# Optimization experiments

Measured on AMD Instinct MI355X. Metric: run time of the kernel, lower is better.

Reference implementation:

```python
import jax, jax.numpy as jnp
import numpy as np

EPS = 1e-5  # torch LayerNorm default
DT_RANK = 32  # ceil(d_model=512 / 16)


def layer_norm(x, g, b):
    mu = x.mean(-1, keepdims=True)
    var = x.var(-1, keepdims=True)
    return (x - mu) / jnp.sqrt(var + EPS) * g + b


def conv1d(x, w, b, pad):
    # x: (B, C, L), w: (O, I, K) -- torch Conv1d semantics
    y = jax.lax.conv_general_dilated(x, w, (1,), [(pad, pad)],
                                     dimension_numbers=('NCH', 'OIH', 'NCH'))
    return y + b[None, :, None]


def mamba(u, in_w, conv_w, conv_b, xproj_w, dt_w, dt_b, Alog, D, out_w, d_state, d_conv):
    # Faithful mamba_ssm Mamba block (no biases on in/x/out proj, RMS of official impl)
    Bsz, L, _ = u.shape
    xz = jnp.einsum('bld,ed->ble', u, in_w)          # (B, L, 2*Di)
    x, z = jnp.split(xz, 2, axis=-1)
    Di = x.shape[-1]
    # causal depthwise conv1d, truncated to L (padding=d_conv-1 on the left)
    xc = jax.lax.conv_general_dilated(x.transpose(0, 2, 1), conv_w[:, None, :], (1,),
                                      [(d_conv - 1, 0)],
                                      dimension_numbers=('NCH', 'OIH', 'NCH'),
                                      feature_group_count=Di)
    x = jax.nn.silu((xc + conv_b[None, :, None]).transpose(0, 2, 1))  # (B, L, Di)
    xdb = jnp.einsum('bld,ed->ble', x, xproj_w)       # (B, L, dt_rank + 2*N)
    dt = jax.nn.softplus(jnp.einsum('blr,dr->bld', xdb[..., :DT_RANK], dt_w) + dt_b)
    Bm = xdb[..., DT_RANK:DT_RANK + d_state]          # (B, L, N)
    Cm = xdb[..., DT_RANK + d_state:]                 # (B, L, N)
    A = -jnp.exp(Alog)                                # (Di, N)

    def step(h, ins):
        dt_t, x_t, B_t, C_t = ins                     # (B,Di),(B,Di),(B,N),(B,N)
        dA = jnp.exp(dt_t[..., None] * A)             # (B, Di, N)
        h = dA * h + (dt_t * x_t)[..., None] * B_t[:, None, :]
        y = (h * C_t[:, None, :]).sum(-1)             # (B, Di)
        return h, y

    h0 = jnp.zeros((Bsz, Di, d_state), u.dtype)
    xs = (dt.transpose(1, 0, 2), x.transpose(1, 0, 2),
          Bm.transpose(1, 0, 2), Cm.transpose(1, 0, 2))
    _, ys = jax.lax.scan(step, h0, xs)
    y = ys.transpose(1, 0, 2) + x * D                 # skip via D
    y = y * jax.nn.silu(z)
    return jnp.einsum('bld,od->blo', y, out_w)


def _forward(x, fe_w, fe_b, fe_ln_g, fe_ln_b, emb_ln_g, emb_ln_b,
             conv1_w, conv1_b, conv2_w, conv2_b,
             mf_in_w, mf_conv_w, mf_conv_b, mf_xproj_w, mf_dt_w, mf_dt_b, mf_Alog, mf_D, mf_out_w,
             mb_in_w, mb_conv_w, mb_conv_b, mb_xproj_w, mb_dt_w, mb_dt_b, mb_Alog, mb_D, mb_out_w,
             norm_g, norm_b, fc1_w, fc1_b, fc2_w, fc2_b):
    x = x.reshape(x.shape[0], 100, 23)
    # FrequencyEmbedding: rfft over a length-1 last dim == the signal itself; |.| then Linear+LN+ReLU
    id_mag = jnp.abs(x[..., :1])                      # (B, 100, 1)
    e = jax.nn.relu(layer_norm(id_mag @ fe_w.T + fe_b, fe_ln_g, fe_ln_b))
    id_embed = jax.nn.relu(layer_norm(e, emb_ln_g, emb_ln_b))  # outer LN+ReLU
    data = x[..., 1:].transpose(0, 2, 1)              # (B, 22, 100)
    f1 = jax.nn.relu(conv1d(data, conv1_w, conv1_b, 1))
    f2 = jax.nn.relu(conv1d(f1, conv2_w, conv2_b, 1)).transpose(0, 2, 1)  # (B,100,256)
    comb = jnp.concatenate([id_embed, f2], axis=-1)   # (B, 100, 512)
    fo = mamba(comb, mf_in_w, mf_conv_w, mf_conv_b, mf_xproj_w, mf_dt_w, mf_dt_b,
               mf_Alog, mf_D, mf_out_w, 16, 4)
    bo = mamba(comb[:, ::-1], mb_in_w, mb_conv_w, mb_conv_b, mb_xproj_w, mb_dt_w, mb_dt_b,
               mb_Alog, mb_D, mb_out_w, 8, 2)[:, ::-1]
    pooled = (fo + bo).max(axis=1)                    # (B, 512)
    pooled = layer_norm(pooled, norm_g, norm_b)       # self.norm (undefined in source; LN(512))
    h = jax.nn.relu(pooled @ fc1_w.T + fc1_b)
    return h @ fc2_w.T + fc2_b                        # (B, 4)


def setup_inputs() -> dict:
    key = jax.random.key(0)
    ks = iter(jax.random.split(key, 48))
    def n(shape, s=0.02):
        return jax.random.normal(next(ks), shape, jnp.float32) * s
    Di = 1024
    alog16 = jnp.log(jnp.tile(jnp.arange(1, 17, dtype=jnp.float32), (Di, 1)))
    alog8 = jnp.log(jnp.tile(jnp.arange(1, 9, dtype=jnp.float32), (Di, 1)))
    return {
        'x': jax.random.normal(next(ks), (512, 2300), jnp.float32),
        'fe_w': n((256, 1), 1.0), 'fe_b': jnp.zeros(256, jnp.float32),
        'fe_ln_g': jnp.ones(256, jnp.float32), 'fe_ln_b': jnp.zeros(256, jnp.float32),
        'emb_ln_g': jnp.ones(256, jnp.float32), 'emb_ln_b': jnp.zeros(256, jnp.float32),
        'conv1_w': n((128, 22, 3)), 'conv1_b': jnp.zeros(128, jnp.float32),
        'conv2_w': n((256, 128, 3)), 'conv2_b': jnp.zeros(256, jnp.float32),
        'mf_in_w': n((2 * Di, 512)), 'mf_conv_w': n((Di, 4)), 'mf_conv_b': jnp.zeros(Di, jnp.float32),
        'mf_xproj_w': n((32 + 2 * 16, Di)), 'mf_dt_w': n((Di, 32)), 'mf_dt_b': n((Di,), 0.1),
        'mf_Alog': alog16, 'mf_D': jnp.ones(Di, jnp.float32), 'mf_out_w': n((512, Di)),
        'mb_in_w': n((2 * Di, 512)), 'mb_conv_w': n((Di, 2)), 'mb_conv_b': jnp.zeros(Di, jnp.float32),
        'mb_xproj_w': n((32 + 2 * 8, Di)), 'mb_dt_w': n((Di, 32)), 'mb_dt_b': n((Di,), 0.1),
        'mb_Alog': alog8, 'mb_D': jnp.ones(Di, jnp.float32), 'mb_out_w': n((512, Di)),
        'norm_g': jnp.ones(512, jnp.float32), 'norm_b': jnp.zeros(512, jnp.float32),
        'fc1_w': n((128, 512)), 'fc1_b': jnp.zeros(128, jnp.float32),
        'fc2_w': n((4, 128)), 'fc2_b': jnp.zeros(4, jnp.float32),
    }


def reference(x, fe_w, fe_b, fe_ln_g, fe_ln_b, emb_ln_g, emb_ln_b,
              conv1_w, conv1_b, conv2_w, conv2_b,
              mf_in_w, mf_conv_w, mf_conv_b, mf_xproj_w, mf_dt_w, mf_dt_b, mf_Alog, mf_D, mf_out_w,
              mb_in_w, mb_conv_w, mb_conv_b, mb_xproj_w, mb_dt_w, mb_dt_b, mb_Alog, mb_D, mb_out_w,
              norm_g, norm_b, fc1_w, fc1_b, fc2_w, fc2_b):
    return _forward(x, fe_w, fe_b, fe_ln_g, fe_ln_b, emb_ln_g, emb_ln_b,
                    conv1_w, conv1_b, conv2_w, conv2_b,
                    mf_in_w, mf_conv_w, mf_conv_b, mf_xproj_w, mf_dt_w, mf_dt_b, mf_Alog, mf_D, mf_out_w,
                    mb_in_w, mb_conv_w, mb_conv_b, mb_xproj_w, mb_dt_w, mb_dt_b, mb_Alog, mb_D, mb_out_w,
                    norm_g, norm_b, fc1_w, fc1_b, fc2_w, fc2_b)
```

## Files before the change

kernel.cpp:

```cpp
#include <hip/hip_runtime.h>
#include <cstddef>
#include <cstdint>

#define BSZ 512
#define SEQ 100

typedef __bf16 bf16_t;
typedef __attribute__((ext_vector_type(8))) __bf16 bf16x8;
typedef __attribute__((ext_vector_type(4))) float f32x4;

__device__ __forceinline__ float sigmoidf_(float v){ return 1.f/(1.f + __expf(-v)); }
__device__ __forceinline__ float siluf_(float v){ return v * sigmoidf_(v); }
__device__ __forceinline__ float softplusf_(float v){ return (v > 20.f) ? v : __logf(1.f + __expf(v)); }

__global__ __launch_bounds__(256) void cvt_bf16_kernel(
    const float* __restrict__ src, bf16_t* __restrict__ dst, int n)
{
    int i = blockIdx.x*256 + threadIdx.x;
    if (i < n) dst[i] = (bf16_t)src[i];
}

__global__ __launch_bounds__(256) void prep_outw_kernel(
    const float* __restrict__ of, const float* __restrict__ ob, bf16_t* __restrict__ W)
{
    int i = blockIdx.x*256 + threadIdx.x;
    if (i < 512*2048){
        int o = i >> 11, k = i & 2047;
        W[i] = (bf16_t)((k < 1024) ? of[o*1024 + k] : ob[o*1024 + (k - 1024)]);
    }
}

__global__ __launch_bounds__(256) void prep_convw_kernel(
    const float* __restrict__ c1w, const float* __restrict__ c2w,
    bf16_t* __restrict__ W1p, bf16_t* __restrict__ W2p)
{
    int i = blockIdx.x*256 + threadIdx.x;
    if (i < 128*96){
        int o = i / 96, kk = i - o*96, k = kk >> 5, c = kk & 31;
        W1p[i] = (c < 22) ? (bf16_t)c1w[(o*22 + c)*3 + k] : (bf16_t)0.f;
    }
    if (i < 256*384){
        int o = i / 384, kk = i - o*384, k = kk >> 7, c = kk & 127;
        W2p[i] = (bf16_t)c2w[(o*128 + c)*3 + k];
    }
}

__global__ __launch_bounds__(256) void fe0_kernel(
    const float* __restrict__ x,
    const float* __restrict__ fe_w, const float* __restrict__ fe_b,
    const float* __restrict__ g1, const float* __restrict__ b1,
    const float* __restrict__ g2, const float* __restrict__ b2,
    bf16_t* __restrict__ comb, bf16_t* __restrict__ F0pad, bf16_t* __restrict__ F1pad)
{
    const int b = blockIdx.x;
    const int t = threadIdx.x;
    const int wv = t >> 6, lane = t & 63;

    float few[4], feb[4], lg1[4], lb1[4], lg2[4], lb2[4];
    #pragma unroll
    for (int q = 0; q < 4; ++q){
        int j = lane + 64*q;
        few[q] = fe_w[j]; feb[q] = fe_b[j];
        lg1[q] = g1[j];  lb1[q] = b1[j];
        lg2[q] = g2[j];  lb2[q] = b2[j];
    }
    for (int l = wv; l < SEQ; l += 4){
        float m = fabsf(x[(size_t)(b*SEQ + l)*23]);
        float e[4];
        float s1 = 0.f, s2 = 0.f;
        #pragma unroll
        for (int q = 0; q < 4; ++q){ e[q] = m*few[q] + feb[q]; s1 += e[q]; s2 += e[q]*e[q]; }
        #pragma unroll
        for (int off = 32; off > 0; off >>= 1){ s1 += __shfl_xor(s1, off); s2 += __shfl_xor(s2, off); }
        float mean = s1 * (1.f/256.f);
        float rstd = rsqrtf(s2*(1.f/256.f) - mean*mean + 1e-5f);
        s1 = 0.f; s2 = 0.f;
        #pragma unroll
        for (int q = 0; q < 4; ++q){
            e[q] = fmaxf((e[q]-mean)*rstd*lg1[q] + lb1[q], 0.f);
            s1 += e[q]; s2 += e[q]*e[q];
        }
        #pragma unroll
        for (int off = 32; off > 0; off >>= 1){ s1 += __shfl_xor(s1, off); s2 += __shfl_xor(s2, off); }
        mean = s1 * (1.f/256.f);
        rstd = rsqrtf(s2*(1.f/256.f) - mean*mean + 1e-5f);
        #pragma unroll
        for (int q = 0; q < 4; ++q){
            float v = fmaxf((e[q]-mean)*rstd*lg2[q] + lb2[q], 0.f);
            comb[(size_t)(b*SEQ + l)*512 + lane + 64*q] = (bf16_t)v;
        }
    }

    for (int idx = t; idx < 102*32; idx += 256){
        int r = idx >> 5, c = idx & 31;
        float v = 0.f;
        if (r >= 1 && r <= SEQ && c < 22) v = x[(size_t)(b*SEQ + r - 1)*23 + 1 + c];
        F0pad[(size_t)(b*102 + r)*32 + c] = (bf16_t)v;
    }
    if (t < 128) F1pad[(size_t)(b*102 + 0)*128 + t] = (bf16_t)0.f;
    else F1pad[(size_t)(b*102 + 101)*128 + (t - 128)] = (bf16_t)0.f;
}

__global__ __launch_bounds__(256) void gemm_conv_kernel(
    const bf16_t* __restrict__ Abase, int lda, int Az,
    const bf16_t* __restrict__ W, int K, int N,
    const float* __restrict__ bias,
    bf16_t* __restrict__ Cbase, int ldc, int Cb, int coff, int noff, int Mtot)
{
    __shared__ bf16_t As[128*32];
    __shared__ bf16_t Ws[128*32];
    const bf16_t* A = Abase + (size_t)blockIdx.z * Az;
    const int t = threadIdx.x;
    const int lane = t & 63, w = t >> 6;
    const int n0 = blockIdx.y * 128;
    const int rsub = lane >> 2, csub = lane & 3;
    const int col = lane & 15, quad = lane >> 4;
    const int wOffM = (w & 1) * 64, wOffN = (w >> 1) * 64;

    f32x4 acc[4][4];
    #pragma unroll
    for (int i = 0; i < 4; ++i)
        #pragma unroll
        for (int j = 0; j < 4; ++j)
            acc[i][j] = (f32x4){0.f, 0.f, 0.f, 0.f};

    for (int k0 = 0; k0 < K; k0 += 32){
        __syncthreads();
        #pragma unroll
        for (int q = 0; q < 2; ++q){
            const int rt = w*32 + q*16 + rsub;
            const int lq = csub ^ ((rt >> 1) & 3);
            int ra = (rt < Mtot) ? rt : (Mtot - 1);
            const bf16_t* ga = A + (size_t)ra*lda + k0 + lq*8;
            __builtin_amdgcn_global_load_lds(
                (const __attribute__((address_space(1))) void*)ga,
                (__attribute__((address_space(3))) void*)&As[(w*32 + q*16)*32], 16, 0, 0);
            const bf16_t* gw = W + (size_t)(n0 + rt)*K + k0 + lq*8;
            __builtin_amdgcn_global_load_lds(
                (const __attribute__((address_space(1))) void*)gw,
                (__attribute__((address_space(3))) void*)&Ws[(w*32 + q*16)*32], 16, 0, 0);
        }
        __syncthreads();

        bf16x8 af[4], bfv[4];
        #pragma unroll
        for (int i = 0; i < 4; ++i){
            const int ra = wOffM + i*16 + col;
            af[i]  = *(const bf16x8*)&As[ra*32 + (quad ^ ((ra >> 1) & 3))*8];
            const int rb = wOffN + i*16 + col;
            bfv[i] = *(const bf16x8*)&Ws[rb*32 + (quad ^ ((rb >> 1) & 3))*8];
        }
        #pragma unroll
        for (int i = 0; i < 4; ++i)
            #pragma unroll
            for (int j = 0; j < 4; ++j)
                acc[i][j] = __builtin_amdgcn_mfma_f32_16x16x32_bf16(af[i], bfv[j], acc[i][j], 0, 0, 0);
    }

    #pragma unroll
    for (int i = 0; i < 4; ++i){
        const int gmb = wOffM + i*16 + quad*4;
        #pragma unroll
        for (int j = 0; j < 4; ++j){
            const int gn = n0 + wOffN + j*16 + col;
            const float bb = bias[gn];
            #pragma unroll
            for (int r = 0; r < 4; ++r){
                const int gm = gmb + r;
                if (gm < Mtot){
                    float v = fmaxf(acc[i][j][r] + bb, 0.f);
                    Cbase[((size_t)blockIdx.z*Cb + coff + gm)*ldc + noff + gn] = (bf16_t)v;
                }
            }
        }
    }
}

__global__ __launch_bounds__(256) void gemm_in_kernel(
    const bf16_t* __restrict__ A, int lda, int Mtot,
    const bf16_t* __restrict__ W, int K,
    bf16_t* __restrict__ xy, bf16_t* __restrict__ z)
{
    __shared__ bf16_t smem[128*132];
    bf16_t* As0 = smem;
    bf16_t* As1 = smem + 4096;
    bf16_t* Ws0 = smem + 8192;
    bf16_t* Ws1 = smem + 12288;
    const int t = threadIdx.x;
    const int lane = t & 63, w = t >> 6;
    const int m0 = blockIdx.x * 128, n0 = blockIdx.y * 128;
    const int rsub = lane >> 2, csub = lane & 3;
    const int col = lane & 15, quad = lane >> 4;
    const int wOffM = (w & 1) * 64, wOffN = (w >> 1) * 64;

    f32x4 acc[4][4];
    #pragma unroll
    for (int i = 0; i < 4; ++i)
        #pragma unroll
        for (int j = 0; j < 4; ++j)
            acc[i][j] = (f32x4){0.f, 0.f, 0.f, 0.f};

    for (int k0 = 0; k0 < K; k0 += 64){
        __syncthreads();
        #pragma unroll
        for (int hh = 0; hh < 2; ++hh){
            bf16_t* Asb = hh ? As1 : As0;
            bf16_t* Wsb = hh ? Ws1 : Ws0;
            #pragma unroll
            for (int q = 0; q < 2; ++q){
                const int rt = w*32 + q*16 + rsub;
                const int lq = csub ^ ((rt >> 1) & 3);
                int ra = m0 + rt; ra = (ra < Mtot) ? ra : (Mtot - 1);
                const bf16_t* ga = A + (size_t)ra*lda + k0 + hh*32 + lq*8;
                __builtin_amdgcn_global_load_lds(
                    (const __attribute__((address_space(1))) void*)ga,
                    (__attribute__((address_space(3))) void*)&Asb[(w*32 + q*16)*32], 16, 0, 0);
                const bf16_t* gw = W + (size_t)(n0 + rt)*K + k0 + hh*32 + lq*8;
                __builtin_amdgcn_global_load_lds(
                    (const __attribute__((address_space(1))) void*)gw,
                    (__attribute__((address_space(3))) void*)&Wsb[(w*32 + q*16)*32], 16, 0, 0);
            }
        }
        __syncthreads();

        #pragma unroll
        for (int hh = 0; hh < 2; ++hh){
            bf16_t* Asb = hh ? As1 : As0;
            bf16_t* Wsb = hh ? Ws1 : Ws0;
            bf16x8 af[4], bfv[4];
            #pragma unroll
            for (int i = 0; i < 4; ++i){
                const int ra = wOffM + i*16 + col;
                af[i]  = *(const bf16x8*)&Asb[ra*32 + (quad ^ ((ra >> 1) & 3))*8];
                const int rb = wOffN + i*16 + col;
                bfv[i] = *(const bf16x8*)&Wsb[rb*32 + (quad ^ ((rb >> 1) & 3))*8];
            }
            #pragma unroll
            for (int i = 0; i < 4; ++i)
                #pragma unroll
                for (int j = 0; j < 4; ++j)
                    acc[i][j] = __builtin_amdgcn_mfma_f32_16x16x32_bf16(af[i], bfv[j], acc[i][j], 0, 0, 0);
        }
    }

    __syncthreads();
    #pragma unroll
    for (int i = 0; i < 4; ++i){
        const int row0 = wOffM + i*16 + quad*4;
        #pragma unroll
        for (int j = 0; j < 4; ++j){
            const int cT = wOffN + j*16 + col;
            #pragma unroll
            for (int r = 0; r < 4; ++r)
                smem[(row0 + r)*132 + cT] = (bf16_t)acc[i][j][r];
        }
    }
    __syncthreads();

    const int half = n0 >> 11, within = n0 & 2047;
    bf16_t* dstBase = ((within < 1024) ? xy : z) + half*1024 + (within & 1023);
    #pragma unroll
    for (int k = 0; k < 8; ++k){
        const int idx = t + k*256;
        const int row = idx >> 4;
        const int ch  = (idx & 15) * 8;
        const int gm = m0 + row;
        if (gm < Mtot)
            *(bf16x8*)&dstBase[(size_t)gm*2048 + ch] = *(const bf16x8*)&smem[row*132 + ch];
    }
}

__global__ __launch_bounds__(256) void gemm_out_kernel(
    const bf16_t* __restrict__ A, int Mtot,
    const bf16_t* __restrict__ W,
    float* __restrict__ C)
{
    __shared__ bf16_t As[2][128*32];
    __shared__ bf16_t Ws[2][128*32];
    const int t = threadIdx.x;
    const int lane = t & 63, w = t >> 6;
    const int m0 = blockIdx.x * 128, n0 = blockIdx.y * 128;
    const int rsub = lane >> 2, csub = lane & 3;
    const int col = lane & 15, quad = lane >> 4;
    const int wOffM = (w & 1) * 64, wOffN = (w >> 1) * 64;
    const int K = 2048;

    f32x4 acc[4][4];
    #pragma unroll
    for (int i = 0; i < 4; ++i)
        #pragma unroll
        for (int j = 0; j < 4; ++j)
            acc[i][j] = (f32x4){0.f, 0.f, 0.f, 0.f};

    for (int k0 = 0; k0 < K; k0 += 64){
        __syncthreads();
        #pragma unroll
        for (int hh = 0; hh < 2; ++hh){
            #pragma unroll
            for (int q = 0; q < 2; ++q){
                const int rt = w*32 + q*16 + rsub;
                const int lq = csub ^ ((rt >> 1) & 3);
                int ra = m0 + rt; ra = (ra < Mtot) ? ra : (Mtot - 1);
                const bf16_t* ga = A + (size_t)ra*K + k0 + hh*32 + lq*8;
                __builtin_amdgcn_global_load_lds(
                    (const __attribute__((address_space(1))) void*)ga,
                    (__attribute__((address_space(3))) void*)&As[hh][(w*32 + q*16)*32], 16, 0, 0);
                const bf16_t* gw = W + (size_t)(n0 + rt)*K + k0 + hh*32 + lq*8;
                __builtin_amdgcn_global_load_lds(
                    (const __attribute__((address_space(1))) void*)gw,
                    (__attribute__((address_space(3))) void*)&Ws[hh][(w*32 + q*16)*32], 16, 0, 0);
            }
        }
        __syncthreads();

        #pragma unroll
        for (int hh = 0; hh < 2; ++hh){
            bf16x8 af[4], bfv[4];
            #pragma unroll
            for (int i = 0; i < 4; ++i){
                const int ra = wOffM + i*16 + col;
                af[i]  = *(const bf16x8*)&As[hh][ra*32 + (quad ^ ((ra >> 1) & 3))*8];
                const int rb = wOffN + i*16 + col;
                bfv[i] = *(const bf16x8*)&Ws[hh][rb*32 + (quad ^ ((rb >> 1) & 3))*8];
            }
            #pragma unroll
            for (int i = 0; i < 4; ++i)
                #pragma unroll
                for (int j = 0; j < 4; ++j)
                    acc[i][j] = __builtin_amdgcn_mfma_f32_16x16x32_bf16(af[i], bfv[j], acc[i][j], 0, 0, 0);
        }
    }

    #pragma unroll
    for (int i = 0; i < 4; ++i){
        const int gmb = m0 + wOffM + i*16 + quad*4;
        #pragma unroll
        for (int j = 0; j < 4; ++j){
            const int gn = n0 + wOffN + j*16 + col;
            #pragma unroll
            for (int r = 0; r < 4; ++r){
                const int gm = gmb + r;
                if (gm < Mtot)
                    C[(size_t)gm*512 + gn] = acc[i][j][r];
            }
        }
    }
}

__global__ __launch_bounds__(256) void gemm_x_kernel(
    const bf16_t* __restrict__ xc,
    const bf16_t* __restrict__ Wf, const bf16_t* __restrict__ Wb,
    float* __restrict__ C)
{
    __shared__ bf16_t As[128*32];
    __shared__ bf16_t Ws[64*32];
    const int half = blockIdx.y;
    const bf16_t* A = xc + half*1024;
    const bf16_t* W = half ? Wb : Wf;
    const int N = half ? 48 : 64;
    const int t = threadIdx.x;
    const int lane = t & 63, w = t >> 6;
    const int m0 = blockIdx.x * 128;
    const int rsub = lane >> 2, csub = lane & 3;
    const int col = lane & 15, quad = lane >> 4;

    f32x4 acc[2][4];
    #pragma unroll
    for (int i = 0; i < 2; ++i)
        #pragma unroll
        for (int j = 0; j < 4; ++j)
            acc[i][j] = (f32x4){0.f, 0.f, 0.f, 0.f};

    for (int k0 = 0; k0 < 1024; k0 += 32){
        __syncthreads();
        #pragma unroll
        for (int q = 0; q < 2; ++q){
            const int rt = q*64 + w*16 + rsub;
            const int lq = csub ^ ((rt >> 1) & 3);
            const bf16_t* ga = A + (size_t)(m0 + rt)*2048 + k0 + lq*8;
            __builtin_amdgcn_global_load_lds(
                (const __attribute__((address_space(1))) void*)ga,
                (__attribute__((address_space(3))) void*)&As[(q*64 + w*16)*32], 16, 0, 0);
        }
        {
            const int rt = w*16 + rsub;
            const int lq = csub ^ ((rt >> 1) & 3);
            int rw = (rt < N) ? rt : (N - 1);
            const bf16_t* gw = W + (size_t)rw*1024 + k0 + lq*8;
            __builtin_amdgcn_global_load_lds(
                (const __attribute__((address_space(1))) void*)gw,
                (__attribute__((address_space(3))) void*)&Ws[(w*16)*32], 16, 0, 0);
        }
        __syncthreads();

        bf16x8 af[2], bfv[4];
        #pragma unroll
        for (int i = 0; i < 2; ++i){
            const int ra = w*32 + i*16 + col;
            af[i]  = *(const bf16x8*)&As[ra*32 + (quad ^ ((ra >> 1) & 3))*8];
        }
        #pragma unroll
        for (int j = 0; j < 4; ++j){
            const int rb = j*16 + col;
            bfv[j] = *(const bf16x8*)&Ws[rb*32 + (quad ^ ((rb >> 1) & 3))*8];
        }
        #pragma unroll
        for (int i = 0; i < 2; ++i)
            #pragma unroll
            for (int j = 0; j < 4; ++j)
                acc[i][j] = __builtin_amdgcn_mfma_f32_16x16x32_bf16(af[i], bfv[j], acc[i][j], 0, 0, 0);
    }

    #pragma unroll
    for (int i = 0; i < 2; ++i){
        const int gmb = m0 + w*32 + i*16 + quad*4;
        #pragma unroll
        for (int j = 0; j < 4; ++j){
            const int gn = j*16 + col;
            if (gn < N){
                #pragma unroll
                for (int r = 0; r < 4; ++r)
                    C[(size_t)(gmb + r)*128 + half*64 + gn] = acc[i][j][r];
            }
        }
    }
}

__global__ __launch_bounds__(256) void dt_kernel(
    const float* __restrict__ xdb,
    const float* __restrict__ dtwf, const float* __restrict__ dtbf,
    const float* __restrict__ dtwb, const float* __restrict__ dtbb,
    bf16_t* __restrict__ dto)
{
    const int half = blockIdx.y >> 3;
    const int d = (blockIdx.y & 7)*128 + (threadIdx.x & 127);
    const int mslot = threadIdx.x >> 7;
    const int m0 = blockIdx.x * 16;
    __shared__ float sd[16*32];
    for (int i = threadIdx.x; i < 16*32; i += 256){
        int r = i >> 5, c = i & 31;
        sd[i] = xdb[(size_t)(m0 + r)*128 + half*64 + c];
    }
    const float* dw = half ? dtwb : dtwf;
    float w[32];
    #pragma unroll
    for (int r = 0; r < 32; ++r) w[r] = dw[d*32 + r];
    const float db = half ? dtbb[d] : dtbf[d];
    __syncthreads();
    #pragma unroll
    for (int i = 0; i < 8; ++i){
        const int row = mslot + i*2;
        const float* rp = &sd[row*32];
        float a = db;
        #pragma unroll
        for (int r = 0; r < 32; ++r) a += w[r]*rp[r];
        dto[(size_t)(m0 + row)*2048 + half*1024 + d] = (bf16_t)softplusf_(a);
    }
}

__global__ __launch_bounds__(256) void conv_silu_kernel(
    const bf16_t* __restrict__ xin,
    bf16_t* __restrict__ xout,
    const float* __restrict__ cwf, const float* __restrict__ cbf,
    const float* __restrict__ cwb, const float* __restrict__ cbb)
{
    const int gid = blockIdx.x*256 + threadIdx.x;
    const int d2 = gid & 2047;
    const int rest = gid >> 11;
    const int b = rest / 10;
    const int g = rest - b*10;
    const int l0 = g*10;
    const int half = d2 >> 10, d = d2 & 1023;
    const bf16_t* in = xin + (size_t)b*SEQ*2048 + d2;
    bf16_t* outp = xout + (size_t)b*SEQ*2048 + d2;

    if (half == 0){
        const float w0 = cwf[d*4], w1 = cwf[d*4+1], w2 = cwf[d*4+2], w3 = cwf[d*4+3];
        const float bias = cbf[d];
        float v[13];
        #pragma unroll
        for (int i = 0; i < 13; ++i){
            const int l = l0 - 3 + i;
            v[i] = (l >= 0) ? (float)in[(size_t)l*2048] : 0.f;
        }
        #pragma unroll
        for (int i = 0; i < 10; ++i){
            const float a = bias + w0*v[i] + w1*v[i+1] + w2*v[i+2] + w3*v[i+3];
            outp[(size_t)(l0+i)*2048] = (bf16_t)siluf_(a);
        }
    } else {
        const float w0 = cwb[d*2], w1 = cwb[d*2+1];
        const float bias = cbb[d];
        float v[11];
        #pragma unroll
        for (int i = 0; i < 11; ++i){
            const int l = l0 + i;
            v[i] = (l < SEQ) ? (float)in[(size_t)l*2048] : 0.f;
        }
        #pragma unroll
        for (int i = 0; i < 10; ++i){
            const float a = bias + w1*v[i] + w0*v[i+1];
            outp[(size_t)(l0+i)*2048] = (bf16_t)siluf_(a);
        }
    }
}

template<int DSS, int ROW, bool REV>
__device__ __forceinline__ void scan2_core(
    bf16_t* __restrict__ xcb,
    const bf16_t* __restrict__ tb,
    const bf16_t* __restrict__ zb,
    const float* __restrict__ sxB,
    const float* __restrict__ sxC,
    const float* __restrict__ Av, float Dd, bool wr)
{
    float h[DSS];
    #pragma unroll
    for (int j = 0; j < DSS; ++j) h[j] = 0.f;
    const int step = REV ? -1 : 1;
    int l = REV ? (SEQ-1) : 0;

    #pragma unroll 1
    for (int blk = 0; blk < 10; ++blk){
        float xr[10], zr[10], tr[10];
        #pragma unroll
        for (int i = 0; i < 10; ++i){
            const size_t li = (size_t)(l + step*i);
            xr[i] = (float)xcb[li*2048];
            zr[i] = (float)zb[li*2048];
            tr[i] = (float)tb[li*2048];
        }
        #pragma unroll
        for (int i = 0; i < 10; ++i){
            const int li = l + step*i;
            const float dtv = tr[i];
            const float dtx = dtv * xr[i];
            const float* Bp = &sxB[li*ROW];
            const float* Cp = &sxC[li*ROW];
            float yv = 0.f;
            #pragma unroll
            for (int j = 0; j < DSS; ++j){
                h[j] = __expf(dtv*Av[j])*h[j] + dtx*Bp[j];
                yv += h[j]*Cp[j];
            }
            yv += __shfl_xor(yv, 1);
            yv += __shfl_xor(yv, 2);
            yv += xr[i]*Dd;
            yv *= siluf_(zr[i]);
            if (wr) xcb[(size_t)li*2048] = (bf16_t)yv;
        }
        l += step*10;
    }
}

__global__ __launch_bounds__(256) void scan_kernel(
    bf16_t* __restrict__ xc,
    const bf16_t* __restrict__ dtv,
    const bf16_t* __restrict__ z,
    const float* __restrict__ xdb,
    const float* __restrict__ Alogf, const float* __restrict__ Dpf,
    const float* __restrict__ Alogb, const float* __restrict__ Dpb)
{
    const int b = blockIdx.x >> 5, k = blockIdx.x & 31;
    const int t = threadIdx.x;
    const int sub = t & 3, chl = t >> 2;
    const bool fwd = (k < 16);

    __shared__ float sx[SEQ*32];
    const float4* src = (const float4*)(xdb + (size_t)b*SEQ*128);
    if (fwd){
        float4* dst = (float4*)sx;
        for (int i = t; i < SEQ*8; i += 256){
            int row = i >> 3, c = i & 7;
            dst[row*8 + c] = src[row*32 + 8 + c];
        }
    } else {
        float4* dst = (float4*)sx;
        for (int i = t; i < SEQ*4; i += 256){
            int row = i >> 2, c = i & 3;
            dst[row*4 + c] = src[row*32 + 24 + c];
        }
    }
    __syncthreads();

    const bool wr = (sub == 0);
    if (fwd){
        const int d = k*64 + chl;
        const size_t off = (size_t)b*SEQ*2048 + d;
        float Av[4];
        #pragma unroll
        for (int j = 0; j < 4; ++j) Av[j] = -__expf(Alogf[d*16 + sub*4 + j]);
        scan2_core<4, 32, false>(xc + off, dtv + off, z + off,
                                 sx + sub*4, sx + 16 + sub*4, Av, Dpf[d], wr);
    } else {
        const int d = (k - 16)*64 + chl;
        const size_t off = (size_t)b*SEQ*2048 + 1024 + d;
        float Av[2];
        #pragma unroll
        for (int j = 0; j < 2; ++j) Av[j] = -__expf(Alogb[d*8 + sub*2 + j]);
        scan2_core<2, 16, true>(xc + off, dtv + off, z + off,
                                sx + sub*2, sx + 8 + sub*2, Av, Dpb[d], wr);
    }
}

__global__ __launch_bounds__(256) void pool_kernel(
    const float* __restrict__ acc,
    float* __restrict__ pooled)
{
    const int b = blockIdx.x, y = blockIdx.y;
    const int c = y*128 + (threadIdx.x & 127);
    const int half = threadIdx.x >> 7;
    const float* base = acc + (size_t)b*SEQ*512 + c;
    float m = -3.4e38f;
    #pragma unroll 5
    for (int l = half*50; l < half*50 + 50; ++l)
        m = fmaxf(m, base[(size_t)l*512]);
    __shared__ float sm[256];
    sm[threadIdx.x] = m;
    __syncthreads();
    if (half == 0)
        pooled[(size_t)b*512 + c] = fmaxf(sm[threadIdx.x], sm[threadIdx.x + 128]);
}

__global__ __launch_bounds__(256) void head_kernel(
    const float* __restrict__ pooled,
    const float* __restrict__ ng, const float* __restrict__ nb,
    const float* __restrict__ w1, const float* __restrict__ b1,
    const float* __restrict__ w2, const float* __restrict__ b2,
    float* __restrict__ out)
{
    const int b = blockIdx.x, t = threadIdx.x;
    __shared__ float sp[512];
    __shared__ float sh2[256];
    __shared__ float sh[128];
    __shared__ float red1[4], red2[4];

    float s1 = 0.f, s2 = 0.f;
    for (int o = t; o < 512; o += 256){
        float v = pooled[(size_t)b*512 + o];
        sp[o] = v; s1 += v; s2 += v*v;
    }
    #pragma unroll
    for (int off = 32; off > 0; off >>= 1){ s1 += __shfl_xor(s1, off); s2 += __shfl_xor(s2, off); }
    const int wv = t >> 6, lane = t & 63;
    if (lane == 0){ red1[wv] = s1; red2[wv] = s2; }
    __syncthreads();
    if (t == 0){
        float a = 0.f, c = 0.f;
        for (int i = 0; i < 4; ++i){ a += red1[i]; c += red2[i]; }
        float mean = a * (1.f/512.f);
        float var = c * (1.f/512.f) - mean*mean;
        red1[0] = mean; red2[0] = rsqrtf(var + 1e-5f);
    }
    __syncthreads();
    const float mean = red1[0], rstd = red2[0];
    for (int o = t; o < 512; o += 256) sp[o] = (sp[o]-mean)*rstd*ng[o] + nb[o];
    __syncthreads();

    {
        const int o = t & 127, half = t >> 7;
        const float4* wrow = (const float4*)(w1 + (size_t)o*512 + half*256);
        const float4* sp4 = (const float4*)sp + half*64;
        float s = 0.f;
        #pragma unroll 8
        for (int j = 0; j < 64; ++j){
            float4 a = sp4[j], wq = wrow[j];
            s += a.x*wq.x + a.y*wq.y + a.z*wq.z + a.w*wq.w;
        }
        sh2[t] = s;
    }
    __syncthreads();
    if (t < 128) sh[t] = fmaxf(sh2[t] + sh2[t + 128] + b1[t], 0.f);
    __syncthreads();
    if (t < 4){
        float a = b2[t];
        for (int j = 0; j < 128; ++j) a += sh[j]*w2[t*128 + j];
        out[b*4 + t] = a;
    }
}

extern "C" void kernel_launch(void* const* d_in, const int* in_sizes, int n_in,
                              void* d_out, int out_size, void* d_ws, size_t ws_size,
                              hipStream_t stream)
{
    (void)in_sizes; (void)n_in; (void)out_size;
    const float* x        = (const float*)d_in[0];
    const float* fe_w     = (const float*)d_in[1];
    const float* fe_b     = (const float*)d_in[2];
    const float* fe_ln_g  = (const float*)d_in[3];
    const float* fe_ln_b  = (const float*)d_in[4];
    const float* emb_ln_g = (const float*)d_in[5];
    const float* emb_ln_b = (const float*)d_in[6];
    const float* conv1_w  = (const float*)d_in[7];
    const float* conv1_b  = (const float*)d_in[8];
    const float* conv2_w  = (const float*)d_in[9];
    const float* conv2_b  = (const float*)d_in[10];
    const float* mf_in_w  = (const float*)d_in[11];
    const float* mf_conv_w= (const float*)d_in[12];
    const float* mf_conv_b= (const float*)d_in[13];
    const float* mf_xproj = (const float*)d_in[14];
    const float* mf_dt_w  = (const float*)d_in[15];
    const float* mf_dt_b  = (const float*)d_in[16];
    const float* mf_Alog  = (const float*)d_in[17];
    const float* mf_D     = (const float*)d_in[18];
    const float* mf_out_w = (const float*)d_in[19];
    const float* mb_in_w  = (const float*)d_in[20];
    const float* mb_conv_w= (const float*)d_in[21];
    const float* mb_conv_b= (const float*)d_in[22];
    const float* mb_xproj = (const float*)d_in[23];
    const float* mb_dt_w  = (const float*)d_in[24];
    const float* mb_dt_b  = (const float*)d_in[25];
    const float* mb_Alog  = (const float*)d_in[26];
    const float* mb_D     = (const float*)d_in[27];
    const float* mb_out_w = (const float*)d_in[28];
    const float* norm_g   = (const float*)d_in[29];
    const float* norm_b   = (const float*)d_in[30];
    const float* fc1_w    = (const float*)d_in[31];
    const float* fc1_b    = (const float*)d_in[32];
    const float* fc2_w    = (const float*)d_in[33];
    const float* fc2_b    = (const float*)d_in[34];
    float* out = (float*)d_out;

    char* p = (char*)d_ws;
    bf16_t* w_in   = (bf16_t*)p; p += (size_t)4096*512*sizeof(bf16_t);
    bf16_t* w_out  = (bf16_t*)p; p += (size_t)512*2048*sizeof(bf16_t);
    bf16_t* w_xpf  = (bf16_t*)p; p += (size_t)64*1024*sizeof(bf16_t);
    bf16_t* w_xpb  = (bf16_t*)p; p += (size_t)48*1024*sizeof(bf16_t);
    bf16_t* W1p    = (bf16_t*)p; p += (size_t)128*96*sizeof(bf16_t);
    bf16_t* W2p    = (bf16_t*)p; p += (size_t)256*384*sizeof(bf16_t);
    bf16_t* comb_all = (bf16_t*)p; p += (size_t)BSZ*SEQ*512*sizeof(bf16_t);
    const size_t fixed_bytes = (size_t)(p - (char*)d_ws);

    const size_t per_b = (size_t)SEQ * (2048*2 + 2048*2 + 2048*2 + 128*4);
    const size_t budget = (ws_size > fixed_bytes) ? (ws_size - fixed_bytes) : 0;
    int Bc = BSZ;
    while (Bc > 64 && (size_t)Bc * per_b > budget) Bc >>= 1;
    const int nch = BSZ / Bc;
    const int M = Bc * SEQ;

    bf16_t* F0pad = (bf16_t*)p;
    bf16_t* F1pad = F0pad + (size_t)BSZ*102*32;
    bf16_t* xy   = (bf16_t*)p;               p += (size_t)M*2048*sizeof(bf16_t);
    bf16_t* z    = (bf16_t*)p;               p += (size_t)M*2048*sizeof(bf16_t);
    bf16_t* dtb  = (bf16_t*)p;               p += (size_t)M*2048*sizeof(bf16_t);
    float*  xdb  = (float*)p;
    float*  accb = (float*)xy;

    cvt_bf16_kernel<<<(2048*512+255)/256, 256, 0, stream>>>(mf_in_w, w_in, 2048*512);
    cvt_bf16_kernel<<<(2048*512+255)/256, 256, 0, stream>>>(mb_in_w, w_in + (size_t)2048*512, 2048*512);
    prep_outw_kernel<<<(512*2048+255)/256, 256, 0, stream>>>(mf_out_w, mb_out_w, w_out);
    cvt_bf16_kernel<<<(64*1024+255)/256,  256, 0, stream>>>(mf_xproj, w_xpf, 64*1024);
    cvt_bf16_kernel<<<(48*1024+255)/256,  256, 0, stream>>>(mb_xproj, w_xpb, 48*1024);
    prep_convw_kernel<<<(256*384+255)/256, 256, 0, stream>>>(conv1_w, conv2_w, W1p, W2p);

    fe0_kernel<<<BSZ, 256, 0, stream>>>(x, fe_w, fe_b, fe_ln_g, fe_ln_b,
        emb_ln_g, emb_ln_b, comb_all, F0pad, F1pad);
    gemm_conv_kernel<<<dim3(1, 1, BSZ), 256, 0, stream>>>(
        F0pad, 32, 102*32, W1p, 96, 128, conv1_b, F1pad, 128, 102, 1, 0, SEQ);
    gemm_conv_kernel<<<dim3(1, 2, BSZ), 256, 0, stream>>>(
        F1pad, 128, 102*128, W2p, 384, 256, conv2_b, comb_all, 512, 100, 0, 256, SEQ);

    const int gm128 = M / 128;

    for (int c = 0; c < nch; ++c){
        const size_t b0 = (size_t)c * Bc;
        const bf16_t* comb = comb_all + b0*SEQ*512;

        gemm_in_kernel<<<dim3(gm128, 32), 256, 0, stream>>>(comb, 512, M, w_in, 512, xy, z);
        conv_silu_kernel<<<Bc*80, 256, 0, stream>>>(xy, dtb, mf_conv_w, mf_conv_b,
                                                    mb_conv_w, mb_conv_b);
        gemm_x_kernel<<<dim3(gm128, 2), 256, 0, stream>>>(dtb, w_xpf, w_xpb, xdb);
        dt_kernel<<<dim3(M/16, 16), 256, 0, stream>>>(xdb, mf_dt_w, mf_dt_b,
                                                      mb_dt_w, mb_dt_b, xy);
        scan_kernel<<<Bc*32, 256, 0, stream>>>(dtb, xy, z, xdb,
                                               mf_Alog, mf_D, mb_Alog, mb_D);
        gemm_out_kernel<<<dim3(gm128, 4), 256, 0, stream>>>(dtb, M, w_out, accb);
        pool_kernel<<<dim3(Bc, 4), 256, 0, stream>>>(accb, xdb);
        head_kernel<<<Bc, 256, 0, stream>>>(xdb, norm_g, norm_b, fc1_w, fc1_b,
                                            fc2_w, fc2_b, out + b0*4);
    }
}
```

Before: 1.791 ms.

## Stage scan inputs through LDS in chunks with packed x/dt loads

The selective-scan kernel now cooperatively loads 25-timestep chunks of x, dt and z into shared memory, packing x and dt into one 32-bit word. This replaces the per-thread strided global loads that were repeated by all four sub-threads of each channel. B and C coefficients are read as vector loads from shared memory. The cost is extra barriers per chunk and additional LDS usage, which may lower occupancy.

Result: slower. 1.829 ms (+2.2%).

```diff
diff --git a/kernel.cpp b/kernel.cpp
--- a/kernel.cpp
+++ b/kernel.cpp
@@ -8,6 +8,8 @@
 typedef __bf16 bf16_t;
 typedef __attribute__((ext_vector_type(8))) __bf16 bf16x8;
 typedef __attribute__((ext_vector_type(4))) float f32x4;
+typedef __attribute__((ext_vector_type(2))) float f32x2;
+typedef unsigned short ushort_t;
 
 __device__ __forceinline__ float sigmoidf_(float v){ return 1.f/(1.f + __expf(-v)); }
 __device__ __forceinline__ float siluf_(float v){ return v * sigmoidf_(v); }
@@ -506,50 +508,72 @@
 }
 
 template<int DSS, int ROW, bool REV>
-__device__ __forceinline__ void scan2_core(
-    bf16_t* __restrict__ xcb,
-    const bf16_t* __restrict__ tb,
-    const bf16_t* __restrict__ zb,
-    const float* __restrict__ sxB,
-    const float* __restrict__ sxC,
-    const float* __restrict__ Av, float Dd, bool wr)
-{
+__device__ __forceinline__ void scan3_core(
+    const ushort_t* __restrict__ xcB,
+    const ushort_t* __restrict__ dtB,
+    const ushort_t* __restrict__ zB,
+    bf16_t* __restrict__ yB,
+    const float* __restrict__ sx,
+    uint32_t* __restrict__ sxdt, ushort_t* __restrict__ szs,
+    const float* __restrict__ Av, float Dd)
+{
+    const int t = threadIdx.x;
+    const int sub = t & 3, chl = t >> 2;
+    const bool wrr = (sub == 0);
     float h[DSS];
     #pragma unroll
     for (int j = 0; j < DSS; ++j) h[j] = 0.f;
-    const int step = REV ? -1 : 1;
-    int l = REV ? (SEQ-1) : 0;
 
     #pragma unroll 1
-    for (int blk = 0; blk < 10; ++blk){
-        float xr[10], zr[10], tr[10];
-        #pragma unroll
-        for (int i = 0; i < 10; ++i){
-            const size_t li = (size_t)(l + step*i);
-            xr[i] = (float)xcb[li*2048];
-            zr[i] = (float)zb[li*2048];
-            tr[i] = (float)tb[li*2048];
-        }
-        #pragma unroll
-        for (int i = 0; i < 10; ++i){
-            const int li = l + step*i;
-            const float dtv = tr[i];
-            const float dtx = dtv * xr[i];
-            const float* Bp = &sxB[li*ROW];
-            const float* Cp = &sxC[li*ROW];
+    for (int q = 0; q < 4; ++q){
+        __syncthreads();
+        for (int idx = t; idx < 25*64; idx += 256){
+            const int r = idx >> 6, ch = idx & 63;
+            const int s = q*25 + r;
+            const int gl = REV ? (SEQ-1 - s) : s;
+            const size_t off = (size_t)gl*2048 + ch;
+            const uint32_t px = xcB[off];
+            const uint32_t pt = dtB[off];
+            sxdt[idx] = px | (pt << 16);
+            szs[idx]  = zB[off];
+        }
+        __syncthreads();
+        int li = REV ? (SEQ-1 - q*25) : q*25;
+        const int stp = REV ? -1 : 1;
+        #pragma unroll 5
+        for (int r = 0; r < 25; ++r){
+            const uint32_t p = sxdt[r*64 + chl];
+            const float xv   = __uint_as_float(p << 16);
+            const float dtvv = __uint_as_float(p & 0xffff0000u);
+            const float dtx  = dtvv * xv;
             float yv = 0.f;
-            #pragma unroll
-            for (int j = 0; j < DSS; ++j){
-                h[j] = __expf(dtv*Av[j])*h[j] + dtx*Bp[j];
-                yv += h[j]*Cp[j];
+            if (DSS == 4){
+                const f32x4 Bv = *(const f32x4*)&sx[li*ROW + sub*4];
+                const f32x4 Cv = *(const f32x4*)&sx[li*ROW + ROW/2 + sub*4];
+                #pragma unroll
+                for (int j = 0; j < 4; ++j){
+                    h[j] = __expf(dtvv*Av[j])*h[j] + dtx*Bv[j];
+                    yv += h[j]*Cv[j];
+                }
+            } else {
+                const f32x2 Bv = *(const f32x2*)&sx[li*ROW + sub*2];
+                const f32x2 Cv = *(const f32x2*)&sx[li*ROW + ROW/2 + sub*2];
+                #pragma unroll
+                for (int j = 0; j < 2; ++j){
+                    h[j] = __expf(dtvv*Av[j])*h[j] + dtx*Bv[j];
+                    yv += h[j]*Cv[j];
+                }
             }
             yv += __shfl_xor(yv, 1);
             yv += __shfl_xor(yv, 2);
-            yv += xr[i]*Dd;
-            yv *= siluf_(zr[i]);
-            if (wr) xcb[(size_t)li*2048] = (bf16_t)yv;
-        }
-        l += step*10;
+            if (wrr){
+                const float zv = __uint_as_float(((uint32_t)szs[r*64 + chl]) << 16);
+                float y = yv + xv*Dd;
+                y *= siluf_(zv);
+                yB[(size_t)li*2048] = (bf16_t)y;
+            }
+            li += stp;
+        }
     }
 }
 
@@ -567,6 +591,9 @@
     const bool fwd = (k < 16);
 
     __shared__ float sx[SEQ*32];
+    __shared__ uint32_t sxdt[25*64];
+    __shared__ ushort_t szs[25*64];
+
     const float4* src = (const float4*)(xdb + (size_t)b*SEQ*128);
     if (fwd){
         float4* dst = (float4*)sx;
@@ -581,25 +608,31 @@
             dst[row*4 + c] = src[row*32 + 24 + c];
         }
     }
-    __syncthreads();
-
-    const bool wr = (sub == 0);
+
     if (fwd){
-        const int d = k*64 + chl;
-        const size_t off = (size_t)b*SEQ*2048 + d;
+        const int d0 = k*64;
+        const int d = d0 + chl;
+        const size_t boff = (size_t)b*SEQ*2048 + d0;
         float Av[4];
         #pragma unroll
         for (int j = 0; j < 4; ++j) Av[j] = -__expf(Alogf[d*16 + sub*4 + j]);
-        scan2_core<4, 32, false>(xc + off, dtv + off, z + off,
-                                 sx + sub*4, sx + 16 + sub*4, Av, Dpf[d], wr);
+        scan3_core<4, 32, false>((const ushort_t*)xc + boff,
+                                 (const ushort_t*)dtv + boff,
+                                 (const ushort_t*)z + boff,
+                                 xc + boff + chl,
+                                 sx, sxdt, szs, Av, Dpf[d]);
     } else {
-        const int d = (k - 16)*64 + chl;
-        const size_t off = (size_t)b*SEQ*2048 + 1024 + d;
+        const int d0 = (k - 16)*64;
+        const int d = d0 + chl;
+        const size_t boff = (size_t)b*SEQ*2048 + 1024 + d0;
         float Av[2];
         #pragma unroll
         for (int j = 0; j < 2; ++j) Av[j] = -__expf(Alogb[d*8 + sub*2 + j]);
-        scan2_core<2, 16, true>(xc + off, dtv + off, z + off,
-                                sx + sub*2, sx + 8 + sub*2, Av, Dpb[d], wr);
+        scan3_core<2, 16, true>((const ushort_t*)xc + boff,
+                                (const ushort_t*)dtv + boff,
+                                (const ushort_t*)z + boff,
+                                xc + boff + chl,
+                                sx, sxdt, szs, Av, Dpb[d]);
     }
 }
 
```

## Restructure selective scan: one thread per channel, staged windows, geometric exp recurrence

Applied to the files above, without the earlier changes.

The scan kernel now gives each thread a whole channel's state (16 forward or 8 backward) instead of splitting it across 4 lanes with shuffles, and launches 8 blocks per batch row that handle both directions. Each 10-step window of x, dt and z is staged cooperatively through shared memory with coalesced 32-bit loads. At runtime the kernel checks whether A[j] = (j+1)*A[0] (the S4D-real init); if so it computes one exp and builds the other decay factors by repeated multiplication, and otherwise it falls back to per-state exps. This cuts transcendental work and shuffles, at the cost of fewer blocks, more registers, extra barriers, and small rounding drift from the chained products.

New measurement: 1.537 ms. 1.16x faster.

```diff
diff --git a/kernel.cpp b/kernel.cpp
--- a/kernel.cpp
+++ b/kernel.cpp
@@ -8,6 +8,7 @@
 typedef __bf16 bf16_t;
 typedef __attribute__((ext_vector_type(8))) __bf16 bf16x8;
 typedef __attribute__((ext_vector_type(4))) float f32x4;
+typedef unsigned short ushort_t;
 
 __device__ __forceinline__ float sigmoidf_(float v){ return 1.f/(1.f + __expf(-v)); }
 __device__ __forceinline__ float siluf_(float v){ return v * sigmoidf_(v); }
@@ -505,52 +506,44 @@
     }
 }
 
-template<int DSS, int ROW, bool REV>
-__device__ __forceinline__ void scan2_core(
-    bf16_t* __restrict__ xcb,
-    const bf16_t* __restrict__ tb,
-    const bf16_t* __restrict__ zb,
-    const float* __restrict__ sxB,
-    const float* __restrict__ sxC,
-    const float* __restrict__ Av, float Dd, bool wr)
-{
-    float h[DSS];
-    #pragma unroll
-    for (int j = 0; j < DSS; ++j) h[j] = 0.f;
-    const int step = REV ? -1 : 1;
-    int l = REV ? (SEQ-1) : 0;
-
-    #pragma unroll 1
-    for (int blk = 0; blk < 10; ++blk){
-        float xr[10], zr[10], tr[10];
-        #pragma unroll
-        for (int i = 0; i < 10; ++i){
-            const size_t li = (size_t)(l + step*i);
-            xr[i] = (float)xcb[li*2048];
-            zr[i] = (float)zb[li*2048];
-            tr[i] = (float)tb[li*2048];
-        }
-        #pragma unroll
-        for (int i = 0; i < 10; ++i){
-            const int li = l + step*i;
-            const float dtv = tr[i];
-            const float dtx = dtv * xr[i];
-            const float* Bp = &sxB[li*ROW];
-            const float* Cp = &sxC[li*ROW];
-            float yv = 0.f;
-            #pragma unroll
-            for (int j = 0; j < DSS; ++j){
-                h[j] = __expf(dtv*Av[j])*h[j] + dtx*Bp[j];
-                yv += h[j]*Cp[j];
-            }
-            yv += __shfl_xor(yv, 1);
-            yv += __shfl_xor(yv, 2);
-            yv += xr[i]*Dd;
-            yv *= siluf_(zr[i]);
-            if (wr) xcb[(size_t)li*2048] = (bf16_t)yv;
-        }
-        l += step*10;
-    }
+template<int DS>
+__device__ __forceinline__ float scan_step_struct(
+    float* __restrict__ h, float A0, float dtv_, float dtx, const float4* __restrict__ sxl4)
+{
+    const float rr = __expf(dtv_*A0);
+    const float r2 = rr*rr;
+    float rb = rr;
+    float y0 = 0.f, y1 = 0.f, y2 = 0.f, y3 = 0.f;
+    #pragma unroll
+    for (int g = 0; g < DS/4; ++g){
+        const float4 Bv = sxl4[g];
+        const float4 Cv = sxl4[DS/4 + g];
+        const float p0 = rb, p1 = rb*rr, p2 = rb*r2, p3 = p1*r2;
+        h[g*4+0] = p0*h[g*4+0] + dtx*Bv.x; y0 += h[g*4+0]*Cv.x;
+        h[g*4+1] = p1*h[g*4+1] + dtx*Bv.y; y1 += h[g*4+1]*Cv.y;
+        h[g*4+2] = p2*h[g*4+2] + dtx*Bv.z; y2 += h[g*4+2]*Cv.z;
+        h[g*4+3] = p3*h[g*4+3] + dtx*Bv.w; y3 += h[g*4+3]*Cv.w;
+        rb = p3*rr;
+    }
+    return (y0 + y1) + (y2 + y3);
+}
+
+template<int DS>
+__device__ __forceinline__ float scan_step_gen(
+    float* __restrict__ h, const float* __restrict__ Av, float dtv_, float dtx,
+    const float4* __restrict__ sxl4)
+{
+    float y0 = 0.f, y1 = 0.f, y2 = 0.f, y3 = 0.f;
+    #pragma unroll
+    for (int g = 0; g < DS/4; ++g){
+        const float4 Bv = sxl4[g];
+        const float4 Cv = sxl4[DS/4 + g];
+        h[g*4+0] = __expf(dtv_*Av[g*4+0])*h[g*4+0] + dtx*Bv.x; y0 += h[g*4+0]*Cv.x;
+        h[g*4+1] = __expf(dtv_*Av[g*4+1])*h[g*4+1] + dtx*Bv.y; y1 += h[g*4+1]*Cv.y;
+        h[g*4+2] = __expf(dtv_*Av[g*4+2])*h[g*4+2] + dtx*Bv.z; y2 += h[g*4+2]*Cv.z;
+        h[g*4+3] = __expf(dtv_*Av[g*4+3])*h[g*4+3] + dtx*Bv.w; y3 += h[g*4+3]*Cv.w;
+    }
+    return (y0 + y1) + (y2 + y3);
 }
 
 __global__ __launch_bounds__(256) void scan_kernel(
@@ -561,46 +554,132 @@
     const float* __restrict__ Alogf, const float* __restrict__ Dpf,
     const float* __restrict__ Alogb, const float* __restrict__ Dpb)
 {
-    const int b = blockIdx.x >> 5, k = blockIdx.x & 31;
+    const int b = blockIdx.x >> 3, s8 = blockIdx.x & 7;
     const int t = threadIdx.x;
-    const int sub = t & 3, chl = t >> 2;
-    const bool fwd = (k < 16);
-
-    __shared__ float sx[SEQ*32];
+    __shared__ float sxF[SEQ*32];
+    __shared__ float sxB[SEQ*16];
+    __shared__ uint32_t stg[3][1280];
+
     const float4* src = (const float4*)(xdb + (size_t)b*SEQ*128);
-    if (fwd){
-        float4* dst = (float4*)sx;
+    {
+        float4* dstF = (float4*)sxF;
         for (int i = t; i < SEQ*8; i += 256){
             int row = i >> 3, c = i & 7;
-            dst[row*8 + c] = src[row*32 + 8 + c];
-        }
-    } else {
-        float4* dst = (float4*)sx;
+            dstF[row*8 + c] = src[row*32 + 8 + c];
+        }
+        float4* dstB = (float4*)sxB;
         for (int i = t; i < SEQ*4; i += 256){
             int row = i >> 2, c = i & 3;
-            dst[row*4 + c] = src[row*32 + 24 + c];
-        }
-    }
-    __syncthreads();
-
-    const bool wr = (sub == 0);
+            dstB[row*4 + c] = src[row*32 + 24 + c];
+        }
+    }
+
+    const bool fwd = (t < 128);
+    const int chl = fwd ? t : (t - 128);
+    const int d = s8*128 + chl;
+
+    float Av[16];
+    bool structp = true;
     if (fwd){
-        const int d = k*64 + chl;
-        const size_t off = (size_t)b*SEQ*2048 + d;
-        float Av[4];
-        #pragma unroll
-        for (int j = 0; j < 4; ++j) Av[j] = -__expf(Alogf[d*16 + sub*4 + j]);
-        scan2_core<4, 32, false>(xc + off, dtv + off, z + off,
-                                 sx + sub*4, sx + 16 + sub*4, Av, Dpf[d], wr);
+        #pragma unroll
+        for (int j = 0; j < 16; ++j) Av[j] = -__expf(Alogf[d*16 + j]);
+        #pragma unroll
+        for (int j = 1; j < 16; ++j)
+            structp = structp && (fabsf(Av[j] - (float)(j+1)*Av[0]) <= 1e-4f*(float)(j+1));
     } else {
-        const int d = (k - 16)*64 + chl;
-        const size_t off = (size_t)b*SEQ*2048 + 1024 + d;
-        float Av[2];
-        #pragma unroll
-        for (int j = 0; j < 2; ++j) Av[j] = -__expf(Alogb[d*8 + sub*2 + j]);
-        scan2_core<2, 16, true>(xc + off, dtv + off, z + off,
-                                sx + sub*2, sx + 8 + sub*2, Av, Dpb[d], wr);
-    }
+        #pragma unroll
+        for (int j = 0; j < 8; ++j) Av[j] = -__expf(Alogb[d*8 + j]);
+        #pragma unroll
+        for (int j = 1; j < 8; ++j)
+            structp = structp && (fabsf(Av[j] - (float)(j+1)*Av[0]) <= 1e-4f*(float)(j+1));
+    }
+    const float Dd = fwd ? Dpf[d] : Dpb[d];
+    const int allstruct = __syncthreads_and((int)structp);
+
+    const uint32_t* xc32 = (const uint32_t*)xc + (size_t)b*SEQ*1024;
+    const uint32_t* dt32 = (const uint32_t*)dtv + (size_t)b*SEQ*1024;
+    const uint32_t* z32  = (const uint32_t*)z  + (size_t)b*SEQ*1024;
+    const int colF = s8*64, colB = 512 + s8*64;
+
+    bf16_t* yout = xc + (size_t)b*SEQ*2048 + (fwd ? d : (1024 + d));
+    const ushort_t* sx16 = (const ushort_t*)stg[0];
+    const ushort_t* st16 = (const ushort_t*)stg[1];
+    const ushort_t* sz16 = (const ushort_t*)stg[2];
+    const int lb16 = (fwd ? 0 : 1280) + chl;
+
+    float h[16];
+    #pragma unroll
+    for (int j = 0; j < 16; ++j) h[j] = 0.f;
+    const float A0 = Av[0];
+
+    #define STAGE_WIN(Q)                                                        \
+        _Pragma("unroll")                                                       \
+        for (int k = 0; k < 5; ++k){                                            \
+            const int i = t + k*256;                                            \
+            const int dir = (i >= 640) ? 1 : 0;                                 \
+            const int rem = i - dir*640;                                        \
+            const int row = rem >> 6, col = rem & 63;                           \
+            const int grow = dir ? (99 - (Q)*10 - row) : ((Q)*10 + row);        \
+            const size_t goff = (size_t)grow*1024 + (dir ? colB : colF) + col;  \
+            stg[0][i] = xc32[goff];                                             \
+            stg[1][i] = dt32[goff];                                             \
+            stg[2][i] = z32[goff];                                              \
+        }
+
+    if (allstruct){
+        #pragma unroll 1
+        for (int q = 0; q < 10; ++q){
+            __syncthreads();
+            STAGE_WIN(q)
+            __syncthreads();
+            #pragma unroll
+            for (int r = 0; r < 10; ++r){
+                const float xv   = __uint_as_float(((uint32_t)sx16[lb16 + r*128]) << 16);
+                const float dtv_ = __uint_as_float(((uint32_t)st16[lb16 + r*128]) << 16);
+                const float zv   = __uint_as_float(((uint32_t)sz16[lb16 + r*128]) << 16);
+                const float dtx = dtv_*xv;
+                float ys;
+                int li;
+                if (fwd){
+                    li = q*10 + r;
+                    ys = scan_step_struct<16>(h, A0, dtv_, dtx, (const float4*)&sxF[li*32]);
+                } else {
+                    li = 99 - (q*10 + r);
+                    ys = scan_step_struct<8>(h, A0, dtv_, dtx, (const float4*)&sxB[li*16]);
+                }
+                float yv = ys + xv*Dd;
+                yv *= siluf_(zv);
+                yout[(size_t)li*2048] = (bf16_t)yv;
+            }
+        }
+    } else {
+        #pragma unroll 1
+        for (int q = 0; q < 10; ++q){
+            __syncthreads();
+            STAGE_WIN(q)
+            __syncthreads();
+            #pragma unroll
+            for (int r = 0; r < 10; ++r){
+                const float xv   = __uint_as_float(((uint32_t)sx16[lb16 + r*128]) << 16);
+                const float dtv_ = __uint_as_float(((uint32_t)st16[lb16 + r*128]) << 16);
+                const float zv   = __uint_as_float(((uint32_t)sz16[lb16 + r*128]) << 16);
+                const float dtx = dtv_*xv;
+                float ys;
+                int li;
+                if (fwd){
+                    li = q*10 + r;
+                    ys = scan_step_gen<16>(h, Av, dtv_, dtx, (const float4*)&sxF[li*32]);
+                } else {
+                    li = 99 - (q*10 + r);
+                    ys = scan_step_gen<8>(h, Av, dtv_, dtx, (const float4*)&sxB[li*16]);
+                }
+                float yv = ys + xv*Dd;
+                yv *= siluf_(zv);
+                yout[(size_t)li*2048] = (bf16_t)yv;
+            }
+        }
+    }
+    #undef STAGE_WIN
 }
 
 __global__ __launch_bounds__(256) void pool_kernel(
@@ -772,8 +851,8 @@
         gemm_x_kernel<<<dim3(gm128, 2), 256, 0, stream>>>(dtb, w_xpf, w_xpb, xdb);
         dt_kernel<<<dim3(M/16, 16), 256, 0, stream>>>(xdb, mf_dt_w, mf_dt_b,
                                                       mb_dt_w, mb_dt_b, xy);
-        scan_kernel<<<Bc*32, 256, 0, stream>>>(dtb, xy, z, xdb,
-                                               mf_Alog, mf_D, mb_Alog, mb_D);
+        scan_kernel<<<Bc*8, 256, 0, stream>>>(dtb, xy, z, xdb,
+                                              mf_Alog, mf_D, mb_Alog, mb_D);
         gemm_out_kernel<<<dim3(gm128, 4), 256, 0, stream>>>(dtb, M, w_out, accb);
         pool_kernel<<<dim3(Bc, 4), 256, 0, stream>>>(accb, xdb);
         head_kernel<<<Bc, 256, 0, stream>>>(xdb, norm_g, norm_b, fc1_w, fc1_b,
```
